# Kernel optimization log

Measured on AMD Instinct MI355X. Metric: run time of the kernel, lower is better.

Reference implementation:

```python
import jax, jax.numpy as jnp
import numpy as np

T, B, I, H = 512, 64, 1024, 1024
G = 4 * H


def setup_inputs() -> dict:
    key = jax.random.key(0)
    k1, k2, k3, k4 = jax.random.split(key, 4)
    scale_in = 1.0 / np.sqrt(I)
    scale_rec = 1.0 / np.sqrt(H)
    return {
        "x": jax.random.normal(k1, (T, B, I), dtype=jnp.float32),
        "h0": jnp.zeros((B, H), dtype=jnp.float32),
        "c0": jnp.zeros((B, H), dtype=jnp.float32),
        "W_in": jax.random.normal(k2, (G, I), dtype=jnp.float32) * scale_in,
        "b": jax.random.normal(k3, (G,), dtype=jnp.float32) * scale_in,
        "W_rec": jax.random.normal(k4, (G, H), dtype=jnp.float32) * scale_rec,
    }


def reference(x, h0, c0, W_in, b, W_rec):
    # Precompute input projection for all timesteps: [T, B, 4H]
    x_proj = jnp.einsum('tbi,gi->tbg', x, W_in) + b

    def step(carry, xp_t):
        h, c = carry
        # subLSTM: all gates are sigmoidal
        gates = jax.nn.sigmoid(xp_t + h @ W_rec.T)  # [B, 4H]
        in_g, out_g, z_g, f_g = jnp.split(gates, 4, axis=-1)
        c_new = c * f_g + z_g - in_g          # subtractive cell update
        h_new = jax.nn.sigmoid(c_new) - out_g  # subtractive output
        return (h_new, c_new), h_new

    (hT, cT), outs = jax.lax.scan(step, (h0, c0), x_proj)
    return outs, hT, cT
```

## Files before the change

kernel.cpp:

```cpp
#include <hip/hip_runtime.h>
#include <hip/hip_bf16.h>
#include <stdint.h>


#define T_STEPS 512
#define NBLK 256

typedef short bf16x8 __attribute__((ext_vector_type(8)));
typedef float f32x4 __attribute__((ext_vector_type(4)));
typedef unsigned int u32x4 __attribute__((ext_vector_type(4)));

#define WS_XBF    0
#define WS_WCAT   67108864
#define WS_HBUF   83886080
#define WS_NEEDED (83886080 + 524288 + 256)

#define LDS_X0   0
#define LDS_H    65536
#define LDS_G    98304
#define LDS_SIZE 106496

__device__ __forceinline__ ushort f2bf(float f) {
  uint32_t u = __float_as_uint(f);
  uint32_t r = (u + 0x7fffu + ((u >> 16) & 1u)) >> 16;
  return (ushort)r;
}

__device__ __forceinline__ float sigmoid_f(float x) {
  float e = __builtin_amdgcn_exp2f(-1.44269504f * x);
  return __builtin_amdgcn_rcpf(1.0f + e);
}

__device__ __forceinline__ u32x4 poll_load16(const unsigned long long* p) {
  u32x4 v;
  asm volatile("global_load_dwordx4 %0, %1, off sc0 sc1"
               : "=v"(v) : "v"(p));
  return v;
}
#define POLL_FENCE() do {                          \
    asm volatile("s_waitcnt vmcnt(0)" ::: "memory"); \
    __builtin_amdgcn_sched_barrier(0);             \
  } while (0)

__global__ void cvt_bf16_kernel(const float* __restrict__ src,
                                ushort* __restrict__ dst, int n4) {
  int i = blockIdx.x * 256 + threadIdx.x;
  if (i >= n4) return;
  float4 v = ((const float4*)src)[i];
  ushort4 o;
  o.x = f2bf(v.x); o.y = f2bf(v.y); o.z = f2bf(v.z); o.w = f2bf(v.w);
  ((ushort4*)dst)[i] = o;
}

__global__ void build_wcat_kernel(const float* __restrict__ w_in,
                                  const float* __restrict__ w_rec,
                                  ushort* __restrict__ wc) {
  int i = blockIdx.x * 256 + threadIdx.x;
  if (i >= (4096 * 2048) / 4) return;
  int col4 = i & 511;
  int g = i >> 9;
  const float* src = (col4 < 256) ? (w_in + (size_t)g * 1024 + col4 * 4)
                                  : (w_rec + (size_t)g * 1024 + (col4 - 256) * 4);
  float4 v = *(const float4*)src;
  ushort4 o;
  o.x = f2bf(v.x); o.y = f2bf(v.y); o.z = f2bf(v.z); o.w = f2bf(v.w);
  ((ushort4*)wc)[i] = o;
}

__global__ void init_hbuf_kernel(const float* __restrict__ h0,
                                 unsigned long long* __restrict__ hb) {
  int i = blockIdx.x * 256 + threadIdx.x;
  if (i >= 65536) return;
  if (i < 32768) {
    int row = i >> 9, u2 = i & 511;
    unsigned lo = f2bf(h0[(size_t)row * 1024 + u2 * 2]);
    unsigned hi = f2bf(h0[(size_t)row * 1024 + u2 * 2 + 1]);
    hb[i] = ((unsigned long long)((hi << 16) | lo) << 32) | 0ull;
  } else {
    hb[i] = 0xFFFFFFFFull;
  }
}

__launch_bounds__(512, 2)
__global__ void sublstm_main(const ushort* __restrict__ xb,
                             const ushort* __restrict__ wc,
                             unsigned long long* __restrict__ hb,
                             const float* __restrict__ c0,
                             const float* __restrict__ bias,
                             float* __restrict__ out) {
  extern __shared__ unsigned char smem[];
  float* gsm = (float*)(smem + LDS_G);

  const int tid  = threadIdx.x;
  const int lane = tid & 63;
  const int wid  = tid >> 6;
  const int gt   = wid >> 1;
  const int kh   = wid & 1;
  const int bid  = blockIdx.x;
  const int b0   = (bid & 3) * 16;
  const int j0   = (bid >> 2) * 16;

  bf16x8 bfrag[32];
  {
    const int row_g = gt * 1024 + j0 + (lane & 15);
    const ushort* wrow = wc + (size_t)row_g * 2048 + kh * 1024 + ((lane >> 4) * 8);
#pragma unroll
    for (int ks = 0; ks < 32; ++ks)
      bfrag[ks] = *(const bf16x8*)(wrow + ks * 32);
  }

  const int bb = tid >> 4, uu = tid & 15;
  float c_reg = 0.f;
  float bias_r0 = 0.f, bias_r1 = 0.f, bias_r2 = 0.f, bias_r3 = 0.f;
  if (tid < 256) {
    c_reg = c0[(size_t)(b0 + bb) * 1024 + j0 + uu];
    bias_r0 = bias[0 * 1024 + j0 + uu];
    bias_r1 = bias[1 * 1024 + j0 + uu];
    bias_r2 = bias[2 * 1024 + j0 + uu];
    bias_r3 = bias[3 * 1024 + j0 + uu];
  }

  const int prow = tid >> 5;
  const int pc   = tid & 31;
  const int arow = lane & 15;
  const int aoff = arow * 2048 + ((lane >> 4) * 16);
  const int aswz = (arow & 7) << 4;
  const int pswz = (prow & 7) << 4;
  const int basew2 = (b0 + prow) * 512 + pc * 2;
  const int hbyte  = prow * 2048 + pc * 8;

  {
    const ushort* xrow = xb + (size_t)b0 * 1024;
#pragma unroll
    for (int j = 0; j < 4; ++j) {
      int L = (tid + j * 512) * 16;
      int row = L >> 11;
      int colb = L & 2047;
      uint4 v = *(const uint4*)(xrow + (size_t)row * 1024 + (colb >> 1));
      *(uint4*)(smem + (L ^ ((row & 7) << 4))) = v;
    }
  }

  for (int t = 0; t < T_STEPS; ++t) {
    {
      const unsigned long long* pb = hb + ((t & 1) << 15) + basew2;
      u32x4 vv[8];
#pragma unroll
      for (int i = 0; i < 8; ++i) vv[i] = poll_load16(pb + i * 64);
      POLL_FENCE();
      for (;;) {
        unsigned np = 0;
#pragma unroll
        for (int i = 0; i < 8; ++i)
          if ((vv[i].x != (unsigned)t) || (vv[i].z != (unsigned)t))
            np |= (1u << i);
        if (!np) break;
        __builtin_amdgcn_s_sleep(1);
#pragma unroll
        for (int i = 0; i < 8; ++i)
          if (np & (1u << i)) vv[i] = poll_load16(pb + i * 64);
        POLL_FENCE();
      }
#pragma unroll
      for (int i = 0; i < 8; ++i) {
        uint2 d; d.x = vv[i].y; d.y = vv[i].w;
        *(uint2*)(smem + LDS_H + ((hbyte + i * 256) ^ pswz)) = d;
      }
    }
    __syncthreads();

    const int abase = (kh ? LDS_H : LDS_X0 + ((t & 1) << 15)) + aoff;
    f32x4 acc0 = {0.f, 0.f, 0.f, 0.f}, acc1 = {0.f, 0.f, 0.f, 0.f};
    f32x4 acc2 = {0.f, 0.f, 0.f, 0.f}, acc3 = {0.f, 0.f, 0.f, 0.f};
#pragma unroll
    for (int ks = 0; ks < 32; ks += 4) {
      bf16x8 a0 = *(const bf16x8*)(smem + ((abase + (ks + 0) * 64) ^ aswz));
      bf16x8 a1 = *(const bf16x8*)(smem + ((abase + (ks + 1) * 64) ^ aswz));
      bf16x8 a2 = *(const bf16x8*)(smem + ((abase + (ks + 2) * 64) ^ aswz));
      bf16x8 a3 = *(const bf16x8*)(smem + ((abase + (ks + 3) * 64) ^ aswz));
      acc0 = __builtin_amdgcn_mfma_f32_16x16x32_bf16(a0, bfrag[ks + 0], acc0, 0, 0, 0);
      acc1 = __builtin_amdgcn_mfma_f32_16x16x32_bf16(a1, bfrag[ks + 1], acc1, 0, 0, 0);
      acc2 = __builtin_amdgcn_mfma_f32_16x16x32_bf16(a2, bfrag[ks + 2], acc2, 0, 0, 0);
      acc3 = __builtin_amdgcn_mfma_f32_16x16x32_bf16(a3, bfrag[ks + 3], acc3, 0, 0, 0);
    }

#pragma unroll
    for (int r = 0; r < 4; ++r)
      gsm[wid * 256 + ((lane >> 4) * 4 + r) * 16 + (lane & 15)] =
          (acc0[r] + acc1[r]) + (acc2[r] + acc3[r]);
    __syncthreads();

    if (tid < 256) {
      float p_in  = gsm[0 * 256 + tid] + gsm[1 * 256 + tid] + bias_r0;
      float p_out = gsm[2 * 256 + tid] + gsm[3 * 256 + tid] + bias_r1;
      float p_z   = gsm[4 * 256 + tid] + gsm[5 * 256 + tid] + bias_r2;
      float p_f   = gsm[6 * 256 + tid] + gsm[7 * 256 + tid] + bias_r3;
      float g_in  = sigmoid_f(p_in);
      float g_out = sigmoid_f(p_out);
      float g_z   = sigmoid_f(p_z);
      float g_f   = sigmoid_f(p_f);
      c_reg = c_reg * g_f + g_z - g_in;
      float h_new = sigmoid_f(c_reg) - g_out;

      unsigned hbits = (unsigned)f2bf(h_new);
      unsigned pv = (unsigned)__shfl_xor((int)hbits, 1);
      if ((uu & 1) == 0) {
        unsigned hi32 = (pv << 16) | hbits;
        int wi = ((1 - (t & 1)) << 15) + (b0 + bb) * 512 + ((j0 + uu) >> 1);
        __hip_atomic_store(&hb[wi],
                           ((unsigned long long)hi32 << 32) |
                               (unsigned long long)(unsigned)(t + 1),
                           __ATOMIC_RELAXED, __HIP_MEMORY_SCOPE_AGENT);
      }
      size_t oidx = (size_t)(b0 + bb) * 1024 + j0 + uu;
      out[(size_t)t * 65536 + oidx] = h_new;
      if (t == T_STEPS - 1) {
        out[(size_t)T_STEPS * 65536 + oidx] = h_new;
        out[(size_t)T_STEPS * 65536 + 65536 + oidx] = c_reg;
      }
    }

    if (t + 1 < T_STEPS) {
      const ushort* xrow = xb + ((size_t)(t + 1) * 64 + b0) * 1024;
      const int xo = ((t + 1) & 1) << 15;
#pragma unroll
      for (int j = 0; j < 4; ++j) {
        int L = (tid + j * 512) * 16;
        int row = L >> 11;
        int colb = L & 2047;
        uint4 v = *(const uint4*)(xrow + (size_t)row * 1024 + (colb >> 1));
        *(uint4*)(smem + xo + (L ^ ((row & 7) << 4))) = v;
      }
    }
  }
}

extern "C" void kernel_launch(void* const* d_in, const int* in_sizes, int n_in,
                              void* d_out, int out_size, void* d_ws, size_t ws_size,
                              hipStream_t stream) {
  const float* x     = (const float*)d_in[0];
  const float* h0    = (const float*)d_in[1];
  const float* c0    = (const float*)d_in[2];
  const float* w_in  = (const float*)d_in[3];
  const float* biasp = (const float*)d_in[4];
  const float* w_rec = (const float*)d_in[5];
  float* outp = (float*)d_out;

  if (ws_size < (size_t)WS_NEEDED) return;

  uint8_t* ws = (uint8_t*)d_ws;
  ushort* xbp = (ushort*)(ws + WS_XBF);
  ushort* wcp = (ushort*)(ws + WS_WCAT);
  unsigned long long* hbp = (unsigned long long*)(ws + WS_HBUF);

  hipFuncSetAttribute(reinterpret_cast<const void*>(sublstm_main),
                      hipFuncAttributeMaxDynamicSharedMemorySize, LDS_SIZE);

  cvt_bf16_kernel<<<32768, 256, 0, stream>>>(x, xbp, 8388608);
  build_wcat_kernel<<<8192, 256, 0, stream>>>(w_in, w_rec, wcp);
  init_hbuf_kernel<<<256, 256, 0, stream>>>(h0, hbp);

  void* kargs[] = { (void*)&xbp, (void*)&wcp, (void*)&hbp,
                    (void*)&c0,  (void*)&biasp, (void*)&outp };
  hipLaunchCooperativeKernel((void*)sublstm_main, dim3(NBLK), dim3(512),
                             kargs, LDS_SIZE, stream);
}
```

Baseline: 1.524 ms.

## Replace step-tagged h exchange with sentinel-based four-slot ring buffer

The hidden-state exchange buffer no longer stores a timestep tag next to each pair of bf16 values. Each 64-bit word now packs four bf16 values, and an all-ones sentinel marks a slot as not ready. Slots rotate over four buffers, and each block clears the slot it will reuse three steps ahead. This halves poll traffic per step and doubles the payload per atomic store. The cost is an extra clearing store, a wait before publishing, and a small risk of misreading a real h value that happens to equal the sentinel.

```diff
diff --git a/kernel.cpp b/kernel.cpp
--- a/kernel.cpp
+++ b/kernel.cpp
@@ -31,15 +31,15 @@
   return __builtin_amdgcn_rcpf(1.0f + e);
 }
 
-__device__ __forceinline__ u32x4 poll_load16(const unsigned long long* p) {
+__device__ __forceinline__ u32x4 poll_load16(const void* p) {
   u32x4 v;
   asm volatile("global_load_dwordx4 %0, %1, off sc0 sc1"
                : "=v"(v) : "v"(p));
   return v;
 }
-#define POLL_FENCE() do {                          \
+#define POLL_FENCE() do {                            \
     asm volatile("s_waitcnt vmcnt(0)" ::: "memory"); \
-    __builtin_amdgcn_sched_barrier(0);             \
+    __builtin_amdgcn_sched_barrier(0);               \
   } while (0)
 
 __global__ void cvt_bf16_kernel(const float* __restrict__ src,
@@ -71,13 +71,17 @@
                                  unsigned long long* __restrict__ hb) {
   int i = blockIdx.x * 256 + threadIdx.x;
   if (i >= 65536) return;
-  if (i < 32768) {
-    int row = i >> 9, u2 = i & 511;
-    unsigned lo = f2bf(h0[(size_t)row * 1024 + u2 * 2]);
-    unsigned hi = f2bf(h0[(size_t)row * 1024 + u2 * 2 + 1]);
-    hb[i] = ((unsigned long long)((hi << 16) | lo) << 32) | 0ull;
+  if (i < 16384) {
+    int row = i >> 8, w = i & 255;
+    const float* s = h0 + (size_t)row * 1024 + w * 4;
+    unsigned long long v = 0;
+    v |= (unsigned long long)f2bf(s[0]);
+    v |= (unsigned long long)f2bf(s[1]) << 16;
+    v |= (unsigned long long)f2bf(s[2]) << 32;
+    v |= (unsigned long long)f2bf(s[3]) << 48;
+    hb[i] = v;
   } else {
-    hb[i] = 0xFFFFFFFFull;
+    hb[i] = ~0ull;
   }
 }
 
@@ -126,8 +130,8 @@
   const int aoff = arow * 2048 + ((lane >> 4) * 16);
   const int aswz = (arow & 7) << 4;
   const int pswz = (prow & 7) << 4;
-  const int basew2 = (b0 + prow) * 512 + pc * 2;
-  const int hbyte  = prow * 2048 + pc * 8;
+  const size_t pollbyte = (size_t)(b0 + prow) * 2048 + pc * 16;
+  const int pubw = ((b0 + bb) * 2048 + (j0 + uu) * 2) >> 3;
 
   {
     const ushort* xrow = xb + (size_t)b0 * 1024;
@@ -143,29 +147,35 @@
 
   for (int t = 0; t < T_STEPS; ++t) {
     {
-      const unsigned long long* pb = hb + ((t & 1) << 15) + basew2;
-      u32x4 vv[8];
-#pragma unroll
-      for (int i = 0; i < 8; ++i) vv[i] = poll_load16(pb + i * 64);
+      const unsigned char* pb =
+          (const unsigned char*)hb + ((size_t)(t & 3) << 17) + pollbyte;
+      u32x4 vv[4];
+#pragma unroll
+      for (int i = 0; i < 4; ++i) vv[i] = poll_load16(pb + i * 512);
       POLL_FENCE();
       for (;;) {
         unsigned np = 0;
 #pragma unroll
-        for (int i = 0; i < 8; ++i)
-          if ((vv[i].x != (unsigned)t) || (vv[i].z != (unsigned)t))
+        for (int i = 0; i < 4; ++i) {
+          if (((vv[i].x & vv[i].y) == 0xFFFFFFFFu) ||
+              ((vv[i].z & vv[i].w) == 0xFFFFFFFFu))
             np |= (1u << i);
+        }
         if (!np) break;
         __builtin_amdgcn_s_sleep(1);
 #pragma unroll
-        for (int i = 0; i < 8; ++i)
-          if (np & (1u << i)) vv[i] = poll_load16(pb + i * 64);
+        for (int i = 0; i < 4; ++i)
+          if (np & (1u << i)) vv[i] = poll_load16(pb + i * 512);
         POLL_FENCE();
       }
 #pragma unroll
-      for (int i = 0; i < 8; ++i) {
-        uint2 d; d.x = vv[i].y; d.y = vv[i].w;
-        *(uint2*)(smem + LDS_H + ((hbyte + i * 256) ^ pswz)) = d;
-      }
+      for (int i = 0; i < 4; ++i)
+        *(u32x4*)(smem + LDS_H + ((prow * 2048 + pc * 16 + i * 512) ^ pswz)) = vv[i];
+    }
+
+    if (tid < 256 && (uu & 3) == 0) {
+      unsigned long long* pz = hb + ((size_t)((t + 3) & 3) << 14) + pubw;
+      __hip_atomic_store(pz, ~0ull, __ATOMIC_RELAXED, __HIP_MEMORY_SCOPE_AGENT);
     }
     __syncthreads();
 
@@ -203,14 +213,15 @@
       float h_new = sigmoid_f(c_reg) - g_out;
 
       unsigned hbits = (unsigned)f2bf(h_new);
-      unsigned pv = (unsigned)__shfl_xor((int)hbits, 1);
-      if ((uu & 1) == 0) {
-        unsigned hi32 = (pv << 16) | hbits;
-        int wi = ((1 - (t & 1)) << 15) + (b0 + bb) * 512 + ((j0 + uu) >> 1);
-        __hip_atomic_store(&hb[wi],
-                           ((unsigned long long)hi32 << 32) |
-                               (unsigned long long)(unsigned)(t + 1),
-                           __ATOMIC_RELAXED, __HIP_MEMORY_SCOPE_AGENT);
+      unsigned p1 = (unsigned)__shfl_xor((int)hbits, 1);
+      unsigned w0 = ((uu & 1) == 0) ? (hbits | (p1 << 16)) : 0u;
+      unsigned w2 = (unsigned)__shfl_xor((int)w0, 2);
+      if ((uu & 3) == 0) {
+        unsigned long long v =
+            (unsigned long long)w0 | ((unsigned long long)w2 << 32);
+        asm volatile("s_waitcnt vmcnt(0)" ::: "memory");
+        unsigned long long* pw = hb + ((size_t)((t + 1) & 3) << 14) + pubw;
+        __hip_atomic_store(pw, v, __ATOMIC_RELAXED, __HIP_MEMORY_SCOPE_AGENT);
       }
       size_t oidx = (size_t)(b0 + bb) * 1024 + j0 + uu;
       out[(size_t)t * 65536 + oidx] = h_new;
```

New measurement: 1.805 ms. +18.4%, slower.

## Split K across all eight waves, each computing all four gates

Applied to the files above, without the earlier changes.

Each wave previously computed one gate over half of K. Now each of the 8 waves takes a 256-wide K slice and computes all four gate tiles. Every A fragment loaded from LDS feeds four MFMAs, which cuts LDS reads per MFMA, and the four accumulators give independent chains. In exchange the cross-wave reduction grows from 2 to 8 partial sums per gate, and the gate scratch area in LDS grows to 128KB, which may limit occupancy at 2 blocks per CU.

```diff
diff --git a/kernel.cpp b/kernel.cpp
--- a/kernel.cpp
+++ b/kernel.cpp
@@ -18,7 +18,7 @@
 #define LDS_X0   0
 #define LDS_H    65536
 #define LDS_G    98304
-#define LDS_SIZE 106496
+#define LDS_SIZE 131072
 
 __device__ __forceinline__ ushort f2bf(float f) {
   uint32_t u = __float_as_uint(f);
@@ -31,15 +31,15 @@
   return __builtin_amdgcn_rcpf(1.0f + e);
 }
 
-__device__ __forceinline__ u32x4 poll_load16(const unsigned long long* p) {
+__device__ __forceinline__ u32x4 poll_load16(const void* p) {
   u32x4 v;
   asm volatile("global_load_dwordx4 %0, %1, off sc0 sc1"
                : "=v"(v) : "v"(p));
   return v;
 }
-#define POLL_FENCE() do {                          \
+#define POLL_FENCE() do {                            \
     asm volatile("s_waitcnt vmcnt(0)" ::: "memory"); \
-    __builtin_amdgcn_sched_barrier(0);             \
+    __builtin_amdgcn_sched_barrier(0);               \
   } while (0)
 
 __global__ void cvt_bf16_kernel(const float* __restrict__ src,
@@ -93,20 +93,21 @@
 
   const int tid  = threadIdx.x;
   const int lane = tid & 63;
-  const int wid  = tid >> 6;
-  const int gt   = wid >> 1;
-  const int kh   = wid & 1;
+  const int w    = tid >> 6;
   const int bid  = blockIdx.x;
   const int b0   = (bid & 3) * 16;
   const int j0   = (bid >> 2) * 16;
 
-  bf16x8 bfrag[32];
+  bf16x8 bfrag[4][8];
   {
-    const int row_g = gt * 1024 + j0 + (lane & 15);
-    const ushort* wrow = wc + (size_t)row_g * 2048 + kh * 1024 + ((lane >> 4) * 8);
-#pragma unroll
-    for (int ks = 0; ks < 32; ++ks)
-      bfrag[ks] = *(const bf16x8*)(wrow + ks * 32);
+    const ushort* wbase =
+        wc + (size_t)(j0 + (lane & 15)) * 2048 + w * 256 + ((lane >> 4) * 8);
+#pragma unroll
+    for (int n = 0; n < 4; ++n)
+#pragma unroll
+      for (int k8 = 0; k8 < 8; ++k8)
+        bfrag[n][k8] =
+            *(const bf16x8*)(wbase + (size_t)n * 2097152 + k8 * 32);
   }
 
   const int bb = tid >> 4, uu = tid & 15;
@@ -123,11 +124,12 @@
   const int prow = tid >> 5;
   const int pc   = tid & 31;
   const int arow = lane & 15;
-  const int aoff = arow * 2048 + ((lane >> 4) * 16);
   const int aswz = (arow & 7) << 4;
   const int pswz = (prow & 7) << 4;
   const int basew2 = (b0 + prow) * 512 + pc * 2;
   const int hbyte  = prow * 2048 + pc * 8;
+  const int aoff = arow * 2048 + ((lane >> 4) * 16);
+  const int abase_nox = (w < 4 ? w * 512 : LDS_H + (w - 4) * 512) + aoff;
 
   {
     const ushort* xrow = xb + (size_t)b0 * 1024;
@@ -169,36 +171,45 @@
     }
     __syncthreads();
 
-    const int abase = (kh ? LDS_H : LDS_X0 + ((t & 1) << 15)) + aoff;
-    f32x4 acc0 = {0.f, 0.f, 0.f, 0.f}, acc1 = {0.f, 0.f, 0.f, 0.f};
-    f32x4 acc2 = {0.f, 0.f, 0.f, 0.f}, acc3 = {0.f, 0.f, 0.f, 0.f};
-#pragma unroll
-    for (int ks = 0; ks < 32; ks += 4) {
-      bf16x8 a0 = *(const bf16x8*)(smem + ((abase + (ks + 0) * 64) ^ aswz));
-      bf16x8 a1 = *(const bf16x8*)(smem + ((abase + (ks + 1) * 64) ^ aswz));
-      bf16x8 a2 = *(const bf16x8*)(smem + ((abase + (ks + 2) * 64) ^ aswz));
-      bf16x8 a3 = *(const bf16x8*)(smem + ((abase + (ks + 3) * 64) ^ aswz));
-      acc0 = __builtin_amdgcn_mfma_f32_16x16x32_bf16(a0, bfrag[ks + 0], acc0, 0, 0, 0);
-      acc1 = __builtin_amdgcn_mfma_f32_16x16x32_bf16(a1, bfrag[ks + 1], acc1, 0, 0, 0);
-      acc2 = __builtin_amdgcn_mfma_f32_16x16x32_bf16(a2, bfrag[ks + 2], acc2, 0, 0, 0);
-      acc3 = __builtin_amdgcn_mfma_f32_16x16x32_bf16(a3, bfrag[ks + 3], acc3, 0, 0, 0);
-    }
-
-#pragma unroll
-    for (int r = 0; r < 4; ++r)
-      gsm[wid * 256 + ((lane >> 4) * 4 + r) * 16 + (lane & 15)] =
-          (acc0[r] + acc1[r]) + (acc2[r] + acc3[r]);
+    const int abase = abase_nox + ((w < 4) ? ((t & 1) << 15) : 0);
+    f32x4 acc0 = {0,0,0,0}, acc1 = {0,0,0,0}, acc2 = {0,0,0,0}, acc3 = {0,0,0,0};
+#pragma unroll
+    for (int k8 = 0; k8 < 8; k8 += 2) {
+      bf16x8 a0 = *(const bf16x8*)(smem + ((abase + k8 * 64) ^ aswz));
+      bf16x8 a1 = *(const bf16x8*)(smem + ((abase + (k8 + 1) * 64) ^ aswz));
+      acc0 = __builtin_amdgcn_mfma_f32_16x16x32_bf16(a0, bfrag[0][k8], acc0, 0, 0, 0);
+      acc1 = __builtin_amdgcn_mfma_f32_16x16x32_bf16(a0, bfrag[1][k8], acc1, 0, 0, 0);
+      acc2 = __builtin_amdgcn_mfma_f32_16x16x32_bf16(a0, bfrag[2][k8], acc2, 0, 0, 0);
+      acc3 = __builtin_amdgcn_mfma_f32_16x16x32_bf16(a0, bfrag[3][k8], acc3, 0, 0, 0);
+      acc0 = __builtin_amdgcn_mfma_f32_16x16x32_bf16(a1, bfrag[0][k8 + 1], acc0, 0, 0, 0);
+      acc1 = __builtin_amdgcn_mfma_f32_16x16x32_bf16(a1, bfrag[1][k8 + 1], acc1, 0, 0, 0);
+      acc2 = __builtin_amdgcn_mfma_f32_16x16x32_bf16(a1, bfrag[2][k8 + 1], acc2, 0, 0, 0);
+      acc3 = __builtin_amdgcn_mfma_f32_16x16x32_bf16(a1, bfrag[3][k8 + 1], acc3, 0, 0, 0);
+    }
+
+#pragma unroll
+    for (int r = 0; r < 4; ++r) {
+      int cell = ((lane >> 4) * 4 + r) * 16 + (lane & 15);
+      gsm[0 * 2048 + w * 256 + cell] = acc0[r];
+      gsm[1 * 2048 + w * 256 + cell] = acc1[r];
+      gsm[2 * 2048 + w * 256 + cell] = acc2[r];
+      gsm[3 * 2048 + w * 256 + cell] = acc3[r];
+    }
     __syncthreads();
 
     if (tid < 256) {
-      float p_in  = gsm[0 * 256 + tid] + gsm[1 * 256 + tid] + bias_r0;
-      float p_out = gsm[2 * 256 + tid] + gsm[3 * 256 + tid] + bias_r1;
-      float p_z   = gsm[4 * 256 + tid] + gsm[5 * 256 + tid] + bias_r2;
-      float p_f   = gsm[6 * 256 + tid] + gsm[7 * 256 + tid] + bias_r3;
-      float g_in  = sigmoid_f(p_in);
-      float g_out = sigmoid_f(p_out);
-      float g_z   = sigmoid_f(p_z);
-      float g_f   = sigmoid_f(p_f);
+      float p0 = bias_r0, p1 = bias_r1, p2 = bias_r2, p3 = bias_r3;
+#pragma unroll
+      for (int w8 = 0; w8 < 8; ++w8) {
+        p0 += gsm[0 * 2048 + w8 * 256 + tid];
+        p1 += gsm[1 * 2048 + w8 * 256 + tid];
+        p2 += gsm[2 * 2048 + w8 * 256 + tid];
+        p3 += gsm[3 * 2048 + w8 * 256 + tid];
+      }
+      float g_in  = sigmoid_f(p0);
+      float g_out = sigmoid_f(p1);
+      float g_z   = sigmoid_f(p2);
+      float g_f   = sigmoid_f(p3);
       c_reg = c_reg * g_f + g_z - g_in;
       float h_new = sigmoid_f(c_reg) - g_out;
 
```

Measured after the change: 2.365 ms. 55.1% more time.

## Pre-swizzle x in bf16 conversion and stream tiles via global_load_lds

Applied to the files above, without the earlier changes.

The conversion kernel now writes x into a pre-swizzled per-block tile layout that matches the LDS layout. The main kernel then copies each next-step x tile with direct global-to-LDS loads issued by the upper four waves right after the MFMA phase, instead of register round-trip loads by all threads after the gate math. This is meant to cut VGPR traffic and take the x prefetch off the critical path of each recurrent step. In exchange it relies on the async LDS writes completing before the next step's reads, which the following barriers are assumed to cover.

```diff
diff --git a/kernel.cpp b/kernel.cpp
--- a/kernel.cpp
+++ b/kernel.cpp
@@ -31,25 +31,40 @@
   return __builtin_amdgcn_rcpf(1.0f + e);
 }
 
-__device__ __forceinline__ u32x4 poll_load16(const unsigned long long* p) {
+__device__ __forceinline__ u32x4 poll_load16(const void* p) {
   u32x4 v;
   asm volatile("global_load_dwordx4 %0, %1, off sc0 sc1"
                : "=v"(v) : "v"(p));
   return v;
 }
-#define POLL_FENCE() do {                          \
+#define POLL_FENCE() do {                            \
     asm volatile("s_waitcnt vmcnt(0)" ::: "memory"); \
-    __builtin_amdgcn_sched_barrier(0);             \
+    __builtin_amdgcn_sched_barrier(0);               \
   } while (0)
 
-__global__ void cvt_bf16_kernel(const float* __restrict__ src,
-                                ushort* __restrict__ dst, int n4) {
+#define GLD_LDS(gp, lp)                                                    \
+  __builtin_amdgcn_global_load_lds(                                        \
+      (const __attribute__((address_space(1))) unsigned int*)(gp),         \
+      (__attribute__((address_space(3))) unsigned int*)(lp), 16, 0, 0)
+
+__global__ void cvt_swz_kernel(const float* __restrict__ src,
+                               ushort* __restrict__ dst) {
   int i = blockIdx.x * 256 + threadIdx.x;
-  if (i >= n4) return;
-  float4 v = ((const float4*)src)[i];
-  ushort4 o;
-  o.x = f2bf(v.x); o.y = f2bf(v.y); o.z = f2bf(v.z); o.w = f2bf(v.w);
-  ((ushort4*)dst)[i] = o;
+  if (i >= 4194304) return;
+  int P    = (i & 2047) * 16;
+  int img  = i >> 11;
+  int row  = P >> 11;
+  int colb = (P & 2047) ^ ((row & 7) << 4);
+  int trow = (img >> 2) * 64 + (img & 3) * 16 + row;
+  const float* s = src + (size_t)trow * 1024 + (colb >> 1);
+  float4 v0 = *(const float4*)s;
+  float4 v1 = *(const float4*)(s + 4);
+  uint4 o;
+  o.x = (unsigned)f2bf(v0.x) | ((unsigned)f2bf(v0.y) << 16);
+  o.y = (unsigned)f2bf(v0.z) | ((unsigned)f2bf(v0.w) << 16);
+  o.z = (unsigned)f2bf(v1.x) | ((unsigned)f2bf(v1.y) << 16);
+  o.w = (unsigned)f2bf(v1.z) | ((unsigned)f2bf(v1.w) << 16);
+  ((uint4*)dst)[i] = o;
 }
 
 __global__ void build_wcat_kernel(const float* __restrict__ w_in,
@@ -90,6 +105,7 @@
                              float* __restrict__ out) {
   extern __shared__ unsigned char smem[];
   float* gsm = (float*)(smem + LDS_G);
+  const unsigned char* xswz = (const unsigned char*)xb;
 
   const int tid  = threadIdx.x;
   const int lane = tid & 63;
@@ -123,22 +139,19 @@
   const int prow = tid >> 5;
   const int pc   = tid & 31;
   const int arow = lane & 15;
-  const int aoff = arow * 2048 + ((lane >> 4) * 16);
   const int aswz = (arow & 7) << 4;
   const int pswz = (prow & 7) << 4;
   const int basew2 = (b0 + prow) * 512 + pc * 2;
   const int hbyte  = prow * 2048 + pc * 8;
-
-  {
-    const ushort* xrow = xb + (size_t)b0 * 1024;
-#pragma unroll
-    for (int j = 0; j < 4; ++j) {
-      int L = (tid + j * 512) * 16;
-      int row = L >> 11;
-      int colb = L & 2047;
-      uint4 v = *(const uint4*)(xrow + (size_t)row * 1024 + (colb >> 1));
-      *(uint4*)(smem + (L ^ ((row & 7) << 4))) = v;
-    }
+  const int aoff   = arow * 2048 + ((lane >> 4) * 16);
+
+  if (wid >= 4) {
+    const unsigned char* sp =
+        xswz + ((size_t)(bid & 3) << 15) + (wid - 4) * 8192 + lane * 16;
+    unsigned char* dp = smem + (wid - 4) * 8192;
+#pragma unroll
+    for (int j = 0; j < 8; ++j)
+      GLD_LDS(sp + j * 1024, dp + j * 1024);
   }
 
   for (int t = 0; t < T_STEPS; ++t) {
@@ -170,8 +183,8 @@
     __syncthreads();
 
     const int abase = (kh ? LDS_H : LDS_X0 + ((t & 1) << 15)) + aoff;
-    f32x4 acc0 = {0.f, 0.f, 0.f, 0.f}, acc1 = {0.f, 0.f, 0.f, 0.f};
-    f32x4 acc2 = {0.f, 0.f, 0.f, 0.f}, acc3 = {0.f, 0.f, 0.f, 0.f};
+    f32x4 acc0 = {0,0,0,0}, acc1 = {0,0,0,0};
+    f32x4 acc2 = {0,0,0,0}, acc3 = {0,0,0,0};
 #pragma unroll
     for (int ks = 0; ks < 32; ks += 4) {
       bf16x8 a0 = *(const bf16x8*)(smem + ((abase + (ks + 0) * 64) ^ aswz));
@@ -188,6 +201,15 @@
     for (int r = 0; r < 4; ++r)
       gsm[wid * 256 + ((lane >> 4) * 4 + r) * 16 + (lane & 15)] =
           (acc0[r] + acc1[r]) + (acc2[r] + acc3[r]);
+
+    if (wid >= 4 && t + 1 < T_STEPS) {
+      const unsigned char* sp = xswz +
+          (((size_t)(t + 1) * 4 + (bid & 3)) << 15) + (wid - 4) * 8192 + lane * 16;
+      unsigned char* dp = smem + (((t + 1) & 1) << 15) + (wid - 4) * 8192;
+#pragma unroll
+      for (int j = 0; j < 8; ++j)
+        GLD_LDS(sp + j * 1024, dp + j * 1024);
+    }
     __syncthreads();
 
     if (tid < 256) {
@@ -219,19 +241,6 @@
         out[(size_t)T_STEPS * 65536 + 65536 + oidx] = c_reg;
       }
     }
-
-    if (t + 1 < T_STEPS) {
-      const ushort* xrow = xb + ((size_t)(t + 1) * 64 + b0) * 1024;
-      const int xo = ((t + 1) & 1) << 15;
-#pragma unroll
-      for (int j = 0; j < 4; ++j) {
-        int L = (tid + j * 512) * 16;
-        int row = L >> 11;
-        int colb = L & 2047;
-        uint4 v = *(const uint4*)(xrow + (size_t)row * 1024 + (colb >> 1));
-        *(uint4*)(smem + xo + (L ^ ((row & 7) << 4))) = v;
-      }
-    }
   }
 }
 
@@ -256,7 +265,7 @@
   hipFuncSetAttribute(reinterpret_cast<const void*>(sublstm_main),
                       hipFuncAttributeMaxDynamicSharedMemorySize, LDS_SIZE);
 
-  cvt_bf16_kernel<<<32768, 256, 0, stream>>>(x, xbp, 8388608);
+  cvt_swz_kernel<<<16384, 256, 0, stream>>>(x, xbp);
   build_wcat_kernel<<<8192, 256, 0, stream>>>(w_in, w_rec, wcp);
   init_hbuf_kernel<<<256, 256, 0, stream>>>(h0, hbp);
 
```

New measurement: 2.706 ms. 1.78x slower.
